# Optimization experiments

Measured on AMD Instinct MI355X. Metric: run time of the kernel, lower is better.

The kernel has to match this reference:

```python
import jax, jax.numpy as jnp
import numpy as np

CLASS_PERIOD = 360
MEAN = True

def setup_inputs() -> dict:
    key = jax.random.key(0)
    k1, k2 = jax.random.split(key)
    preds = jax.random.normal(k1, (131072, CLASS_PERIOD), dtype=jnp.float32)
    labels = jax.random.randint(k2, (131072,), 0, CLASS_PERIOD, dtype=jnp.int64 if jax.config.jax_enable_x64 else jnp.int32)
    return {"preds": preds, "labels": labels}

def reference(preds, labels):
    # per-row L1 normalization: x_i / sum(|x_i|)
    l1 = jnp.sum(jnp.abs(preds), axis=-1, keepdims=True)        # [B, 1]
    scaled = preds / l1                                          # [B, C]
    logp = jax.nn.log_softmax(scaled, axis=-1)                   # [B, C]
    gathered = jnp.take_along_axis(logp, labels[:, None], axis=-1)[:, 0]  # [B]
    if MEAN:
        # original: (one_hot * logp).mean() per instance = logp[label] / C
        loss = -jnp.sum(gathered) / CLASS_PERIOD
    else:
        loss = -jnp.sum(gathered)
    return loss.reshape(1)
```

## Files before the change

kernel.cpp:

```cpp
#include <hip/hip_runtime.h>
#include <hip/hip_bf16.h>
#include <math.h>

#define NROWS 131072
#define NCOLS 360
#define ROWS_PER_WAVE 8
#define NWAVES (NROWS / ROWS_PER_WAVE)
#define NBLOCKS (NWAVES / 4)

typedef float f32x4 __attribute__((ext_vector_type(4)));

__global__ __launch_bounds__(256) void viewpoint_row_kernel(
    const float* __restrict__ preds,
    const int* __restrict__ labels,
    float* __restrict__ partial)
{
    const int wave = threadIdx.x >> 6;
    const int lane = threadIdx.x & 63;
    const int wgid = blockIdx.x * 4 + wave;
    const bool have2 = lane < (90 - 64);

    float gacc = 0.f;

    #pragma unroll
    for (int r = 0; r < ROWS_PER_WAVE; r += 2) {
        const int rowA = r * NWAVES + wgid;
        const int rowB = (r + 1) * NWAVES + wgid;
        const f32x4* pA = (const f32x4*)(preds + (size_t)rowA * NCOLS);
        const f32x4* pB = (const f32x4*)(preds + (size_t)rowB * NCOLS);

        f32x4 a0 = __builtin_nontemporal_load(pA + lane);
        f32x4 b0 = __builtin_nontemporal_load(pB + lane);
        f32x4 a1 = {0.f, 0.f, 0.f, 0.f};
        f32x4 b1 = {0.f, 0.f, 0.f, 0.f};
        if (have2) {
            a1 = __builtin_nontemporal_load(pA + 64 + lane);
            b1 = __builtin_nontemporal_load(pB + 64 + lane);
        }

        float sA = (fabsf(a0.x) + fabsf(a0.y)) + (fabsf(a0.z) + fabsf(a0.w))
                 + ((fabsf(a1.x) + fabsf(a1.y)) + (fabsf(a1.z) + fabsf(a1.w)));
        float sB = (fabsf(b0.x) + fabsf(b0.y)) + (fabsf(b0.z) + fabsf(b0.w))
                 + ((fabsf(b1.x) + fabsf(b1.y)) + (fabsf(b1.z) + fabsf(b1.w)));

        #pragma unroll
        for (int off = 32; off > 0; off >>= 1) {
            sA += __shfl_xor(sA, off);
            sB += __shfl_xor(sB, off);
        }

        const float invA = __builtin_amdgcn_rcpf(sA);
        const float invB = __builtin_amdgcn_rcpf(sB);

        float eA = (__expf(a0.x * invA) + __expf(a0.y * invA))
                 + (__expf(a0.z * invA) + __expf(a0.w * invA));
        float eB = (__expf(b0.x * invB) + __expf(b0.y * invB))
                 + (__expf(b0.z * invB) + __expf(b0.w * invB));
        if (have2) {
            eA += (__expf(a1.x * invA) + __expf(a1.y * invA))
                + (__expf(a1.z * invA) + __expf(a1.w * invA));
            eB += (__expf(b1.x * invB) + __expf(b1.y * invB))
                + (__expf(b1.z * invB) + __expf(b1.w * invB));
        }
        #pragma unroll
        for (int off = 32; off > 0; off >>= 1) {
            eA += __shfl_xor(eA, off);
            eB += __shfl_xor(eB, off);
        }

        {
            const int lab = labels[rowA];
            const int f4i = lab >> 2, c = lab & 3;
            const f32x4 src = (f4i < 64) ? a0 : a1;
            const int owner = (f4i < 64) ? f4i : (f4i - 64);
            const float v = (c == 0) ? src.x : (c == 1) ? src.y
                          : (c == 2) ? src.z : src.w;
            gacc += __shfl(v, owner) * invA - __logf(eA);
        }
        {
            const int lab = labels[rowB];
            const int f4i = lab >> 2, c = lab & 3;
            const f32x4 src = (f4i < 64) ? b0 : b1;
            const int owner = (f4i < 64) ? f4i : (f4i - 64);
            const float v = (c == 0) ? src.x : (c == 1) ? src.y
                          : (c == 2) ? src.z : src.w;
            gacc += __shfl(v, owner) * invB - __logf(eB);
        }
    }

    __shared__ float sh[4];
    if (lane == 0) sh[wave] = gacc;
    __syncthreads();
    if (threadIdx.x == 0)
        partial[blockIdx.x] = sh[0] + sh[1] + sh[2] + sh[3];
}

__global__ __launch_bounds__(256) void viewpoint_final_kernel(
    const float* __restrict__ partial, float* __restrict__ out, int n4)
{
    const f32x4* p4 = (const f32x4*)partial;
    float s = 0.f;
    for (int i = threadIdx.x; i < n4; i += 256) {
        f32x4 v = p4[i];
        s += (v.x + v.y) + (v.z + v.w);
    }
    #pragma unroll
    for (int off = 32; off > 0; off >>= 1) s += __shfl_xor(s, off);
    __shared__ float sh[4];
    if ((threadIdx.x & 63) == 0) sh[threadIdx.x >> 6] = s;
    __syncthreads();
    if (threadIdx.x == 0)
        out[0] = -(sh[0] + sh[1] + sh[2] + sh[3]) * (1.0f / (float)NCOLS);
}

extern "C" void kernel_launch(void* const* d_in, const int* in_sizes, int n_in,
                              void* d_out, int out_size, void* d_ws, size_t ws_size,
                              hipStream_t stream) {
    const float* preds  = (const float*)d_in[0];
    const int*   labels = (const int*)d_in[1];
    float* out = (float*)d_out;
    float* partial = (float*)d_ws;

    viewpoint_row_kernel<<<NBLOCKS, 256, 0, stream>>>(preds, labels, partial);
    viewpoint_final_kernel<<<1, 256, 0, stream>>>(partial, out, NBLOCKS / 4);
}
```

Before: 247.2 us.

## Fuse final reduction via last-block atomic counter and prefetch next row pair

```diff
diff --git a/kernel.cpp b/kernel.cpp
--- a/kernel.cpp
+++ b/kernel.cpp
@@ -10,10 +10,12 @@
 
 typedef float f32x4 __attribute__((ext_vector_type(4)));
 
-__global__ __launch_bounds__(256) void viewpoint_row_kernel(
+__global__ __launch_bounds__(256) void viewpoint_fused_kernel(
     const float* __restrict__ preds,
     const int* __restrict__ labels,
-    float* __restrict__ partial)
+    float* __restrict__ partial,
+    unsigned int* __restrict__ counter,
+    float* __restrict__ out)
 {
     const int wave = threadIdx.x >> 6;
     const int lane = threadIdx.x & 63;
@@ -22,20 +24,33 @@
 
     float gacc = 0.f;
 
+    const f32x4* pA = (const f32x4*)(preds + (size_t)(0 * NWAVES + wgid) * NCOLS);
+    const f32x4* pB = (const f32x4*)(preds + (size_t)(1 * NWAVES + wgid) * NCOLS);
+    f32x4 a0 = __builtin_nontemporal_load(pA + lane);
+    f32x4 b0 = __builtin_nontemporal_load(pB + lane);
+    f32x4 a1 = {0.f, 0.f, 0.f, 0.f};
+    f32x4 b1 = {0.f, 0.f, 0.f, 0.f};
+    if (have2) {
+        a1 = __builtin_nontemporal_load(pA + 64 + lane);
+        b1 = __builtin_nontemporal_load(pB + 64 + lane);
+    }
+
     #pragma unroll
     for (int r = 0; r < ROWS_PER_WAVE; r += 2) {
         const int rowA = r * NWAVES + wgid;
         const int rowB = (r + 1) * NWAVES + wgid;
-        const f32x4* pA = (const f32x4*)(preds + (size_t)rowA * NCOLS);
-        const f32x4* pB = (const f32x4*)(preds + (size_t)rowB * NCOLS);
 
-        f32x4 a0 = __builtin_nontemporal_load(pA + lane);
-        f32x4 b0 = __builtin_nontemporal_load(pB + lane);
-        f32x4 a1 = {0.f, 0.f, 0.f, 0.f};
-        f32x4 b1 = {0.f, 0.f, 0.f, 0.f};
-        if (have2) {
-            a1 = __builtin_nontemporal_load(pA + 64 + lane);
-            b1 = __builtin_nontemporal_load(pB + 64 + lane);
+        f32x4 na0 = {0.f, 0.f, 0.f, 0.f}, nb0 = {0.f, 0.f, 0.f, 0.f};
+        f32x4 na1 = {0.f, 0.f, 0.f, 0.f}, nb1 = {0.f, 0.f, 0.f, 0.f};
+        if (r + 2 < ROWS_PER_WAVE) {
+            const f32x4* nA = (const f32x4*)(preds + (size_t)((r + 2) * NWAVES + wgid) * NCOLS);
+            const f32x4* nB = (const f32x4*)(preds + (size_t)((r + 3) * NWAVES + wgid) * NCOLS);
+            na0 = __builtin_nontemporal_load(nA + lane);
+            nb0 = __builtin_nontemporal_load(nB + lane);
+            if (have2) {
+                na1 = __builtin_nontemporal_load(nA + 64 + lane);
+                nb1 = __builtin_nontemporal_load(nB + 64 + lane);
+            }
         }
 
         float sA = (fabsf(a0.x) + fabsf(a0.y)) + (fabsf(a0.z) + fabsf(a0.w))
@@ -86,31 +101,39 @@
                           : (c == 2) ? src.z : src.w;
             gacc += __shfl(v, owner) * invB - __logf(eB);
         }
+
+        a0 = na0; a1 = na1; b0 = nb0; b1 = nb1;
     }
 
     __shared__ float sh[4];
+    __shared__ bool amLast;
     if (lane == 0) sh[wave] = gacc;
     __syncthreads();
-    if (threadIdx.x == 0)
+    if (threadIdx.x == 0) {
         partial[blockIdx.x] = sh[0] + sh[1] + sh[2] + sh[3];
-}
+        __threadfence();
+        const unsigned int prev = atomicAdd(counter, 1u);
+        amLast = (prev == (unsigned int)(NBLOCKS - 1));
+    }
+    __syncthreads();
 
-__global__ __launch_bounds__(256) void viewpoint_final_kernel(
-    const float* __restrict__ partial, float* __restrict__ out, int n4)
-{
-    const f32x4* p4 = (const f32x4*)partial;
-    float s = 0.f;
-    for (int i = threadIdx.x; i < n4; i += 256) {
-        f32x4 v = p4[i];
-        s += (v.x + v.y) + (v.z + v.w);
+    if (amLast) {
+        __threadfence();
+        const int n4 = NBLOCKS / 4;
+        float s = 0.f;
+        for (int i = threadIdx.x; i < n4; i += 256) {
+            volatile const float* pp = partial + (size_t)i * 4;
+            const float x = pp[0], y = pp[1], z = pp[2], w = pp[3];
+            s += (x + y) + (z + w);
+        }
+        #pragma unroll
+        for (int off = 32; off > 0; off >>= 1) s += __shfl_xor(s, off);
+        __shared__ float sh2[4];
+        if (lane == 0) sh2[wave] = s;
+        __syncthreads();
+        if (threadIdx.x == 0)
+            out[0] = -(sh2[0] + sh2[1] + sh2[2] + sh2[3]) * (1.0f / (float)NCOLS);
     }
-    #pragma unroll
-    for (int off = 32; off > 0; off >>= 1) s += __shfl_xor(s, off);
-    __shared__ float sh[4];
-    if ((threadIdx.x & 63) == 0) sh[threadIdx.x >> 6] = s;
-    __syncthreads();
-    if (threadIdx.x == 0)
-        out[0] = -(sh[0] + sh[1] + sh[2] + sh[3]) * (1.0f / (float)NCOLS);
 }
 
 extern "C" void kernel_launch(void* const* d_in, const int* in_sizes, int n_in,
@@ -120,7 +143,9 @@
     const int*   labels = (const int*)d_in[1];
     float* out = (float*)d_out;
     float* partial = (float*)d_ws;
+    unsigned int* counter = (unsigned int*)((char*)d_ws + NBLOCKS * sizeof(float));
 
-    viewpoint_row_kernel<<<NBLOCKS, 256, 0, stream>>>(preds, labels, partial);
-    viewpoint_final_kernel<<<1, 256, 0, stream>>>(partial, out, NBLOCKS / 4);
+    hipMemsetAsync(counter, 0, sizeof(unsigned int), stream);
+
+    viewpoint_fused_kernel<<<NBLOCKS, 256, 0, stream>>>(preds, labels, partial, counter, out);
 }
```

After: 407.2 us. 1.65x slower.
